# Optimization experiments

Measured on AMD Instinct MI355X. Metric: run time of the kernel, lower is better.

Reference implementation:

```python
import jax, jax.numpy as jnp
import numpy as np

G = 32          # grid size passed to FlashKAN
K_DEG = 3       # cubic B-splines
LO, HI = -3.0, 3.0

def make_knots():
    h = (HI - LO) / G
    # extended uniform knot vector: G + 2k + 1 knots -> G + k = 35 cubic basis fns
    return jnp.asarray(np.linspace(LO - K_DEG * h, HI + K_DEG * h, G + 2 * K_DEG + 1), jnp.float32)

def bspline_basis(x, knots):
    # Cox-de Boor, vectorized over all leading dims; loop only over degree (3 iters)
    xe = jnp.clip(x, LO, HI - 1e-4)[..., None]
    b = ((xe >= knots[:-1]) & (xe < knots[1:])).astype(x.dtype)  # degree-0 indicators
    for d in range(1, K_DEG + 1):
        left = (xe - knots[:-(d + 1)]) / (knots[d:-1] - knots[:-(d + 1)]) * b[..., :-1]
        right = (knots[d + 1:] - xe) / (knots[d + 1:] - knots[1:-d]) * b[..., 1:]
        b = left + right
    return b  # [..., E, G+K_DEG]

def kan(x, w_base, w_sp, knots):
    # FlashKAN layer: SiLU base branch + B-spline branch
    base = jax.nn.silu(x) @ w_base                          # [..., E] @ [E, O]
    spline = jnp.einsum('bleg,ego->blo', bspline_basis(x, knots), w_sp)
    return base + spline

def reference(query, key, value, wq_base, wq_sp, wk_base, wk_sp, wv_base, wv_sp):
    B, L, E = query.shape
    S = key.shape[-2]
    H = 8
    Dh = E // H
    knots = make_knots()
    Q = kan(query, wq_base, wq_sp, knots).reshape(B, L, H, Dh).transpose(0, 2, 1, 3)
    K = kan(key, wk_base, wk_sp, knots).reshape(B, S, H, Dh).transpose(0, 2, 1, 3)
    V = kan(value, wv_base, wv_sp, knots).reshape(B, S, H, Dh).transpose(0, 2, 1, 3)
    # no softmax, dropout p=0 -> (Q @ K^T) @ V == Q @ (K^T @ V), use O(L*d^2) form
    KtV = jnp.einsum('bhsd,bhse->bhde', K, V)               # [B,H,Dh,Dh]
    out = jnp.einsum('bhld,bhde->bhle', Q, KtV)             # [B,H,L,Dh]
    return out.transpose(0, 2, 1, 3).reshape(B, L, E)

def setup_inputs():
    key = jax.random.key(0)
    ks = jax.random.split(key, 9)
    B, L, E, NB = 2, 1024, 512, G + K_DEG
    sp_scale = 0.1 / np.sqrt(E)
    base_scale = 1.0 / np.sqrt(E)
    return {
        'query': jax.random.normal(ks[0], (B, L, E), jnp.float32),
        'key': jax.random.normal(ks[1], (B, L, E), jnp.float32),
        'value': jax.random.normal(ks[2], (B, L, E), jnp.float32),
        'wq_base': jax.random.normal(ks[3], (E, E), jnp.float32) * base_scale,
        'wq_sp': jax.random.normal(ks[4], (E, NB, E), jnp.float32) * sp_scale,
        'wk_base': jax.random.normal(ks[5], (E, E), jnp.float32) * base_scale,
        'wk_sp': jax.random.normal(ks[6], (E, NB, E), jnp.float32) * sp_scale,
        'wv_base': jax.random.normal(ks[7], (E, E), jnp.float32) * base_scale,
        'wv_sp': jax.random.normal(ks[8], (E, NB, E), jnp.float32) * sp_scale,
    }
```

## Files before the change

kernel.cpp:

```cpp
#include <hip/hip_runtime.h>
#include <hip/hip_bf16.h>
#include <stdint.h>

#define E_DIM 512
#define GNB   35
#define KSP   17920
#define KAUG  18432
#define MTOK  2048
#define BKW   128
#define NWIN  144
#define WINB  140
#define BM    128
#define BN    128

typedef __attribute__((ext_vector_type(8))) short  short8;
typedef __attribute__((ext_vector_type(4))) short  short4v;
typedef __attribute__((ext_vector_type(4))) float  floatx4;

__device__ __forceinline__ short f2bf(float f) {
  __hip_bfloat16 h = __float2bfloat16(f);
  return *reinterpret_cast<short*>(&h);
}
__device__ __forceinline__ float silu_f(float x) { return x / (1.0f + __expf(-x)); }

__device__ __forceinline__ void gload_lds16(const void* g, void* l) {
  typedef const __attribute__((address_space(1))) void* gp_t;
  typedef __attribute__((address_space(3))) void* lp_t;
  __builtin_amdgcn_global_load_lds((gp_t)g, (lp_t)l, 16, 0, 0);
}

__device__ __forceinline__ int kofs(int sl) { return ((sl >> 2) << 5) + ((sl & 3) << 3); }

__global__ __launch_bounds__(256) void wconv_kernel(
    const float* __restrict__ wq_sp, const float* __restrict__ wq_base,
    const float* __restrict__ wk_sp, const float* __restrict__ wk_base,
    const float* __restrict__ wv_sp, const float* __restrict__ wv_base,
    __hip_bfloat16* __restrict__ waugT)
{
  __shared__ float tile[64][65];
  const int tz = blockIdx.z;
  const float* wsp = tz == 0 ? wq_sp : (tz == 1 ? wk_sp : wv_sp);
  const float* wb  = tz == 0 ? wq_base : (tz == 1 ? wk_base : wv_base);
  const int k0 = blockIdx.x * 64;
  const int o0 = blockIdx.y * 64;
  const int t  = threadIdx.x;
  const float* srcb = (k0 < KSP) ? wsp + (size_t)k0 * E_DIM
                                 : wb + (size_t)(k0 - KSP) * E_DIM;
#pragma unroll
  for (int it = 0; it < 4; ++it) {
    int idx = it * 256 + t;
    int r = idx >> 4, c4 = (idx & 15) * 4;
    floatx4 v = *(const floatx4*)&srcb[(size_t)r * E_DIM + o0 + c4];
    tile[r][c4] = v.x; tile[r][c4 + 1] = v.y;
    tile[r][c4 + 2] = v.z; tile[r][c4 + 3] = v.w;
  }
  __syncthreads();
  __hip_bfloat16* dst = waugT + (size_t)tz * E_DIM * KAUG;
#pragma unroll
  for (int it = 0; it < 4; ++it) {
    int idx = it * 256 + t;
    int ro = idx >> 4, kc = (idx & 15) * 4;
    short4v s;
    s.x = f2bf(tile[kc][ro]);     s.y = f2bf(tile[kc + 1][ro]);
    s.z = f2bf(tile[kc + 2][ro]); s.w = f2bf(tile[kc + 3][ro]);
    *(short4v*)&dst[(size_t)(o0 + ro) * KAUG + k0 + kc] = s;
  }
}

template<int MODE>
__global__ __launch_bounds__(256) void kan_gemm(
    const float* __restrict__ q, const float* __restrict__ k_in,
    const float* __restrict__ v, const __hip_bfloat16* __restrict__ waugT,
    const float* __restrict__ wq_sp, const float* __restrict__ wq_base,
    const float* __restrict__ wk_sp, const float* __restrict__ wk_base,
    const float* __restrict__ wv_sp, const float* __restrict__ wv_base,
    float* __restrict__ C)
{
  __shared__ char pA[32768];
  __shared__ char pB[32768];

  const int bid = blockIdx.x;
  const int lid = (bid & 7) * 96 + (bid >> 3);
  const int mx = lid & 15;
  const int ny = (lid >> 4) & 3;
  const int z  = lid >> 6;
  const int tz = z >> 2;
  const int ks = z & 3;

  const float* X = tz == 0 ? q : (tz == 1 ? k_in : v);
  const float* Wsp = tz == 0 ? wq_sp : (tz == 1 ? wk_sp : wv_sp);
  const float* Wb  = tz == 0 ? wq_base : (tz == 1 ? wk_base : wv_base);
  const char* WTb = (const char*)(waugT + (size_t)tz * E_DIM * KAUG);
  float* Cout = C + (size_t)tz * MTOK * E_DIM;

  const int m0 = mx * BM;
  const int n0 = ny * BN;
  const int t = threadIdx.x;
  const int lane = t & 63, wid = t >> 6;
  const int wm = wid >> 1, wn = wid & 1;
  const int fr = lane & 15, kg = lane >> 4;

  floatx4 acc[4][4];
  const floatx4 zf = {0.f, 0.f, 0.f, 0.f};
#pragma unroll
  for (int i = 0; i < 4; ++i)
#pragma unroll
    for (int j = 0; j < 4; ++j) acc[i][j] = zf;

  const int colt = t & 127;
  const int slhi = t >> 7;

  const int w_lo = ks * (NWIN / 4), w_hi = w_lo + (NWIN / 4);
  for (int win = w_lo; win < w_hi; ++win) {
    const int k0 = win * BKW;
    const bool spline = (win < WINB);
    __syncthreads();

    if (MODE == 0) {
#pragma unroll
      for (int p = 0; p < 8; ++p) {
        const int sl = 2 * p + slhi;
        size_t goff = ((size_t)(n0 + colt) * KAUG + k0 + kofs(sl)) * 2;
        gload_lds16(WTb + goff, pB + p * 4096 + t * 16);
      }
    } else {
      const float* Wrow = spline ? Wsp : Wb;
      const int koff0 = spline ? k0 : k0 - KSP;
      const int g  = t & 31;
      const int rg = t >> 5;
#pragma unroll
      for (int p = 0; p < 4; ++p) {
        const int r0 = (p * 8 + rg) * 4;
        const int sl = ((r0 >> 5) << 2) | ((r0 >> 3) & 3);
        float rv[4][4];
#pragma unroll
        for (int j = 0; j < 4; ++j) {
          const float* src = &Wrow[(size_t)(koff0 + r0 + j) * E_DIM + n0 + g];
#pragma unroll
          for (int j2 = 0; j2 < 4; ++j2) rv[j][j2] = src[32 * j2];
        }
#pragma unroll
        for (int j2 = 0; j2 < 4; ++j2) {
          const int nloc = g + 32 * j2;
          short4v sv;
          sv.x = f2bf(rv[0][j2]); sv.y = f2bf(rv[1][j2]);
          sv.z = f2bf(rv[2][j2]); sv.w = f2bf(rv[3][j2]);
          *(short4v*)&pB[sl * 2048 + nloc * 16 + (r0 & 7) * 2] = sv;
        }
      }
    }

    if (spline) {
      const int4 z4 = make_int4(0, 0, 0, 0);
#pragma unroll
      for (int p = 0; p < 8; ++p) ((int4*)pA)[p * 256 + t] = z4;
      asm volatile("s_waitcnt lgkmcnt(0)" ::: "memory");
      __builtin_amdgcn_s_barrier();
      const int elo = k0 / GNB;
      int ehi = (k0 + BKW - 1) / GNB; if (ehi > 511) ehi = 511;
      const int ne = ehi - elo + 1;
      const int npairs = BM * ne;
      for (int p = t; p < npairs; p += 256) {
        int m, ei;
        if (ne == 4) { m = p >> 2; ei = p & 3; }
        else         { m = (p * 52429) >> 18; ei = p - m * 5; }
        const int e = elo + ei;
        float x = X[(size_t)(m0 + m) * E_DIM + e];
        x = fminf(fmaxf(x, -3.0f), 3.0f - 1e-4f);
        float u = (x + 3.0f) * (16.0f / 3.0f);
        int ii = (int)u; ii = ii > 31 ? 31 : ii;
        float tt = u - (float)ii;
        float omt = 1.0f - tt;
        float t2 = tt * tt, t3 = t2 * tt;
        float w4[4];
        w4[0] = omt * omt * omt * (1.0f / 6.0f);
        w4[1] = (3.0f * t3 - 6.0f * t2 + 4.0f) * (1.0f / 6.0f);
        w4[2] = (-3.0f * t3 + 3.0f * t2 + 3.0f * tt + 1.0f) * (1.0f / 6.0f);
        w4[3] = t3 * (1.0f / 6.0f);
        const int c = e * GNB + ii - k0;
#pragma unroll
        for (int j = 0; j < 4; ++j) {
          const int k = c + j;
          if (k >= 0 && k < BKW) {
            const int sl = ((k >> 5) << 2) | ((k >> 3) & 3);
            *(short*)&pA[sl * 2048 + m * 16 + (k & 7) * 2] = f2bf(w4[j]);
          }
        }
      }
    } else {
      const int e0 = k0 - KSP;
#pragma unroll
      for (int p = 0; p < 8; ++p) {
        const int id = p * 256 + t;
        const int m = id & 127, sl = id >> 7;
        const float* xs = &X[(size_t)(m0 + m) * E_DIM + e0 + kofs(sl)];
        floatx4 a = *(const floatx4*)xs;
        floatx4 b = *(const floatx4*)(xs + 4);
        short8 pk;
        pk[0] = f2bf(silu_f(a.x)); pk[1] = f2bf(silu_f(a.y));
        pk[2] = f2bf(silu_f(a.z)); pk[3] = f2bf(silu_f(a.w));
        pk[4] = f2bf(silu_f(b.x)); pk[5] = f2bf(silu_f(b.y));
        pk[6] = f2bf(silu_f(b.z)); pk[7] = f2bf(silu_f(b.w));
        *(short8*)&pA[sl * 2048 + m * 16] = pk;
      }
    }
    asm volatile("s_waitcnt vmcnt(0) lgkmcnt(0)" ::: "memory");
    __builtin_amdgcn_s_barrier();

    const int arow = (wm * 64 + fr) * 16;
    const int brow = (wn * 64 + fr) * 16;
    const int sbase = kg * 2048;
#pragma unroll
    for (int kc = 0; kc < 4; ++kc) {
      const int so = sbase + kc * 8192;
      short8 af[4], bfv[4];
#pragma unroll
      for (int fm = 0; fm < 4; ++fm)
        af[fm] = *(const short8*)&pA[so + arow + fm * 256];
#pragma unroll
      for (int fn = 0; fn < 4; ++fn)
        bfv[fn] = *(const short8*)&pB[so + brow + fn * 256];
#pragma unroll
      for (int fm = 0; fm < 4; ++fm)
#pragma unroll
        for (int fn = 0; fn < 4; ++fn)
          acc[fm][fn] = __builtin_amdgcn_mfma_f32_16x16x32_bf16(
              af[fm], bfv[fn], acc[fm][fn], 0, 0, 0);
    }
  }

  const int rowb = kg * 4;
#pragma unroll
  for (int fm = 0; fm < 4; ++fm)
#pragma unroll
    for (int fn = 0; fn < 4; ++fn)
#pragma unroll
      for (int r = 0; r < 4; ++r)
        atomicAdd(&Cout[(size_t)(m0 + wm * 64 + fm * 16 + rowb + r) * E_DIM
                        + (n0 + wn * 64 + fn * 16 + fr)],
                  acc[fm][fn][r]);
}

__global__ __launch_bounds__(256) void ktv_kernel(const float* __restrict__ C,
                                                  float* __restrict__ KtV)
{
  __shared__ float Ks[64][64];
  __shared__ float Vs[64][64];
  const int sc = blockIdx.x, bh = blockIdx.y;
  const int b = bh >> 3, h = bh & 7;
  const int t = threadIdx.x;
  const size_t base = ((size_t)(b * 1024 + sc * 64)) * E_DIM + h * 64;
  const float* Kp = C + (size_t)MTOK * E_DIM + base;
  const float* Vp = C + (size_t)2 * MTOK * E_DIM + base;
#pragma unroll
  for (int p = 0; p < 16; ++p) {
    int idx = p * 256 + t;
    int r = idx >> 6, c = idx & 63;
    Ks[r][c] = Kp[(size_t)r * E_DIM + c];
    Vs[r][c] = Vp[(size_t)r * E_DIM + c];
  }
  __syncthreads();
  const int d0 = (t & 15) * 4, e0 = (t >> 4) * 4;
  float acc[4][4] = {};
  for (int s = 0; s < 64; ++s) {
    float4 kv = *(const float4*)&Ks[s][d0];
    float4 vv = *(const float4*)&Vs[s][e0];
    float ka[4] = {kv.x, kv.y, kv.z, kv.w};
    float va[4] = {vv.x, vv.y, vv.z, vv.w};
#pragma unroll
    for (int i = 0; i < 4; ++i)
#pragma unroll
      for (int j = 0; j < 4; ++j) acc[i][j] = __fmaf_rn(ka[i], va[j], acc[i][j]);
  }
  float* dst = KtV + (size_t)bh * 4096;
#pragma unroll
  for (int i = 0; i < 4; ++i)
#pragma unroll
    for (int j = 0; j < 4; ++j)
      atomicAdd(&dst[(d0 + i) * 64 + (e0 + j)], acc[i][j]);
}

__global__ __launch_bounds__(256) void qktv_kernel(const float* __restrict__ C,
                                                   const float* __restrict__ KtV,
                                                   float* __restrict__ out)
{
  __shared__ float Qs[128][64];
  __shared__ float Ms[64][64];
  const int lt = blockIdx.x, bh = blockIdx.y;
  const int b = bh >> 3, h = bh & 7;
  const int t = threadIdx.x;
  const float* Qp = C + ((size_t)(b * 1024 + lt * 128)) * E_DIM + h * 64;
#pragma unroll
  for (int p = 0; p < 32; ++p) {
    int idx = p * 256 + t;
    Qs[idx >> 6][idx & 63] = Qp[(size_t)(idx >> 6) * E_DIM + (idx & 63)];
  }
#pragma unroll
  for (int p = 0; p < 16; ++p) {
    int idx = p * 256 + t;
    Ms[idx >> 6][idx & 63] = KtV[(size_t)bh * 4096 + idx];
  }
  __syncthreads();
  const int e0 = (t & 15) * 4;
  const int l0 = (t >> 4) * 8;
  float acc[8][4] = {};
  for (int d = 0; d < 64; ++d) {
    float4 mv = *(const float4*)&Ms[d][e0];
    float ma[4] = {mv.x, mv.y, mv.z, mv.w};
#pragma unroll
    for (int i = 0; i < 8; ++i) {
      float qv = Qs[l0 + i][d];
#pragma unroll
      for (int j = 0; j < 4; ++j) acc[i][j] = __fmaf_rn(qv, ma[j], acc[i][j]);
    }
  }
  float* op = out + ((size_t)(b * 1024 + lt * 128)) * E_DIM + h * 64;
#pragma unroll
  for (int i = 0; i < 8; ++i)
#pragma unroll
    for (int j = 0; j < 4; ++j)
      op[(size_t)(l0 + i) * E_DIM + (e0 + j)] = acc[i][j];
}

extern "C" void kernel_launch(void* const* d_in, const int* in_sizes, int n_in,
                              void* d_out, int out_size, void* d_ws, size_t ws_size,
                              hipStream_t stream) {
  const float* q   = (const float*)d_in[0];
  const float* k   = (const float*)d_in[1];
  const float* v   = (const float*)d_in[2];
  const float* wqb = (const float*)d_in[3];
  const float* wqs = (const float*)d_in[4];
  const float* wkb = (const float*)d_in[5];
  const float* wks = (const float*)d_in[6];
  const float* wvb = (const float*)d_in[7];
  const float* wvs = (const float*)d_in[8];

  char* ws = (char*)d_ws;
  const size_t WAUG_BYTES = (size_t)3 * E_DIM * KAUG * sizeof(__hip_bfloat16);
  const size_t C_BYTES    = (size_t)3 * MTOK * E_DIM * sizeof(float);
  const size_t KTV_BYTES  = (size_t)16 * 64 * 64 * sizeof(float);
  const bool full = ws_size >= WAUG_BYTES + C_BYTES + KTV_BYTES;

  float* C;
  float* KtV;
  __hip_bfloat16* waugT = (__hip_bfloat16*)ws;
  if (full) { C = (float*)(ws + WAUG_BYTES); KtV = (float*)(ws + WAUG_BYTES + C_BYTES); }
  else      { C = (float*)ws;                KtV = (float*)(ws + C_BYTES); }

  hipMemsetAsync(C, 0, C_BYTES, stream);
  hipMemsetAsync(KtV, 0, KTV_BYTES, stream);

  if (full) {
    wconv_kernel<<<dim3(KAUG / 64, E_DIM / 64, 3), 256, 0, stream>>>(
        wqs, wqb, wks, wkb, wvs, wvb, waugT);
    kan_gemm<0><<<dim3(768), 256, 0, stream>>>(
        q, k, v, waugT, wqs, wqb, wks, wkb, wvs, wvb, C);
  } else {
    kan_gemm<1><<<dim3(768), 256, 0, stream>>>(
        q, k, v, waugT, wqs, wqb, wks, wkb, wvs, wvb, C);
  }
  ktv_kernel<<<dim3(16, 16), 256, 0, stream>>>(C, KtV);
  qktv_kernel<<<dim3(8, 16), 256, 0, stream>>>(C, KtV, (float*)d_out);
}
```

Baseline: 440.8 us.

## Drop weight pre-conversion pass and software-pipeline KAN GEMM with double-buffered LDS

```diff
diff --git a/kernel.cpp b/kernel.cpp
--- a/kernel.cpp
+++ b/kernel.cpp
@@ -7,14 +7,13 @@
 #define KSP   17920
 #define KAUG  18432
 #define MTOK  2048
-#define BKW   128
-#define NWIN  144
-#define WINB  140
+#define BKW   64
+#define NWIN  288
+#define WINB  280
 #define BM    128
 #define BN    128
 
 typedef __attribute__((ext_vector_type(8))) short  short8;
-typedef __attribute__((ext_vector_type(4))) short  short4v;
 typedef __attribute__((ext_vector_type(4))) float  floatx4;
 
 __device__ __forceinline__ short f2bf(float f) {
@@ -23,61 +22,17 @@
 }
 __device__ __forceinline__ float silu_f(float x) { return x / (1.0f + __expf(-x)); }
 
-__device__ __forceinline__ void gload_lds16(const void* g, void* l) {
-  typedef const __attribute__((address_space(1))) void* gp_t;
-  typedef __attribute__((address_space(3))) void* lp_t;
-  __builtin_amdgcn_global_load_lds((gp_t)g, (lp_t)l, 16, 0, 0);
-}
-
 __device__ __forceinline__ int kofs(int sl) { return ((sl >> 2) << 5) + ((sl & 3) << 3); }
 
-__global__ __launch_bounds__(256) void wconv_kernel(
-    const float* __restrict__ wq_sp, const float* __restrict__ wq_base,
-    const float* __restrict__ wk_sp, const float* __restrict__ wk_base,
-    const float* __restrict__ wv_sp, const float* __restrict__ wv_base,
-    __hip_bfloat16* __restrict__ waugT)
-{
-  __shared__ float tile[64][65];
-  const int tz = blockIdx.z;
-  const float* wsp = tz == 0 ? wq_sp : (tz == 1 ? wk_sp : wv_sp);
-  const float* wb  = tz == 0 ? wq_base : (tz == 1 ? wk_base : wv_base);
-  const int k0 = blockIdx.x * 64;
-  const int o0 = blockIdx.y * 64;
-  const int t  = threadIdx.x;
-  const float* srcb = (k0 < KSP) ? wsp + (size_t)k0 * E_DIM
-                                 : wb + (size_t)(k0 - KSP) * E_DIM;
-#pragma unroll
-  for (int it = 0; it < 4; ++it) {
-    int idx = it * 256 + t;
-    int r = idx >> 4, c4 = (idx & 15) * 4;
-    floatx4 v = *(const floatx4*)&srcb[(size_t)r * E_DIM + o0 + c4];
-    tile[r][c4] = v.x; tile[r][c4 + 1] = v.y;
-    tile[r][c4 + 2] = v.z; tile[r][c4 + 3] = v.w;
-  }
-  __syncthreads();
-  __hip_bfloat16* dst = waugT + (size_t)tz * E_DIM * KAUG;
-#pragma unroll
-  for (int it = 0; it < 4; ++it) {
-    int idx = it * 256 + t;
-    int ro = idx >> 4, kc = (idx & 15) * 4;
-    short4v s;
-    s.x = f2bf(tile[kc][ro]);     s.y = f2bf(tile[kc + 1][ro]);
-    s.z = f2bf(tile[kc + 2][ro]); s.w = f2bf(tile[kc + 3][ro]);
-    *(short4v*)&dst[(size_t)(o0 + ro) * KAUG + k0 + kc] = s;
-  }
-}
-
-template<int MODE>
-__global__ __launch_bounds__(256) void kan_gemm(
+__global__ __launch_bounds__(256, 2) void kan_gemm(
     const float* __restrict__ q, const float* __restrict__ k_in,
-    const float* __restrict__ v, const __hip_bfloat16* __restrict__ waugT,
+    const float* __restrict__ v,
     const float* __restrict__ wq_sp, const float* __restrict__ wq_base,
     const float* __restrict__ wk_sp, const float* __restrict__ wk_base,
     const float* __restrict__ wv_sp, const float* __restrict__ wv_base,
     float* __restrict__ C)
 {
-  __shared__ char pA[32768];
-  __shared__ char pB[32768];
+  __shared__ char lds[65536];
 
   const int bid = blockIdx.x;
   const int lid = (bid & 7) * 96 + (bid >> 3);
@@ -87,10 +42,9 @@
   const int tz = z >> 2;
   const int ks = z & 3;
 
-  const float* X = tz == 0 ? q : (tz == 1 ? k_in : v);
+  const float* X   = tz == 0 ? q : (tz == 1 ? k_in : v);
   const float* Wsp = tz == 0 ? wq_sp : (tz == 1 ? wk_sp : wv_sp);
   const float* Wb  = tz == 0 ? wq_base : (tz == 1 ? wk_base : wv_base);
-  const char* WTb = (const char*)(waugT + (size_t)tz * E_DIM * KAUG);
   float* Cout = C + (size_t)tz * MTOK * E_DIM;
 
   const int m0 = mx * BM;
@@ -99,6 +53,7 @@
   const int lane = t & 63, wid = t >> 6;
   const int wm = wid >> 1, wn = wid & 1;
   const int fr = lane & 15, kg = lane >> 4;
+  const int gB = t & 31, slB = t >> 5;
 
   floatx4 acc[4][4];
   const floatx4 zf = {0.f, 0.f, 0.f, 0.f};
@@ -107,119 +62,157 @@
 #pragma unroll
     for (int j = 0; j < 4; ++j) acc[i][j] = zf;
 
-  const int colt = t & 127;
-  const int slhi = t >> 7;
-
   const int w_lo = ks * (NWIN / 4), w_hi = w_lo + (NWIN / 4);
-  for (int win = w_lo; win < w_hi; ++win) {
-    const int k0 = win * BKW;
-    const bool spline = (win < WINB);
-    __syncthreads();
-
-    if (MODE == 0) {
-#pragma unroll
-      for (int p = 0; p < 8; ++p) {
-        const int sl = 2 * p + slhi;
-        size_t goff = ((size_t)(n0 + colt) * KAUG + k0 + kofs(sl)) * 2;
-        gload_lds16(WTb + goff, pB + p * 4096 + t * 16);
-      }
-    } else {
-      const float* Wrow = spline ? Wsp : Wb;
-      const int koff0 = spline ? k0 : k0 - KSP;
-      const int g  = t & 31;
-      const int rg = t >> 5;
-#pragma unroll
-      for (int p = 0; p < 4; ++p) {
-        const int r0 = (p * 8 + rg) * 4;
-        const int sl = ((r0 >> 5) << 2) | ((r0 >> 3) & 3);
-        float rv[4][4];
-#pragma unroll
-        for (int j = 0; j < 4; ++j) {
-          const float* src = &Wrow[(size_t)(koff0 + r0 + j) * E_DIM + n0 + g];
-#pragma unroll
-          for (int j2 = 0; j2 < 4; ++j2) rv[j][j2] = src[32 * j2];
-        }
-#pragma unroll
-        for (int j2 = 0; j2 < 4; ++j2) {
-          const int nloc = g + 32 * j2;
-          short4v sv;
-          sv.x = f2bf(rv[0][j2]); sv.y = f2bf(rv[1][j2]);
-          sv.z = f2bf(rv[2][j2]); sv.w = f2bf(rv[3][j2]);
-          *(short4v*)&pB[sl * 2048 + nloc * 16 + (r0 & 7) * 2] = sv;
-        }
-      }
-    }
-
-    if (spline) {
-      const int4 z4 = make_int4(0, 0, 0, 0);
-#pragma unroll
-      for (int p = 0; p < 8; ++p) ((int4*)pA)[p * 256 + t] = z4;
-      asm volatile("s_waitcnt lgkmcnt(0)" ::: "memory");
-      __builtin_amdgcn_s_barrier();
-      const int elo = k0 / GNB;
-      int ehi = (k0 + BKW - 1) / GNB; if (ehi > 511) ehi = 511;
-      const int ne = ehi - elo + 1;
-      const int npairs = BM * ne;
-      for (int p = t; p < npairs; p += 256) {
-        int m, ei;
-        if (ne == 4) { m = p >> 2; ei = p & 3; }
-        else         { m = (p * 52429) >> 18; ei = p - m * 5; }
-        const int e = elo + ei;
-        float x = X[(size_t)(m0 + m) * E_DIM + e];
-        x = fminf(fmaxf(x, -3.0f), 3.0f - 1e-4f);
-        float u = (x + 3.0f) * (16.0f / 3.0f);
-        int ii = (int)u; ii = ii > 31 ? 31 : ii;
-        float tt = u - (float)ii;
-        float omt = 1.0f - tt;
-        float t2 = tt * tt, t3 = t2 * tt;
-        float w4[4];
-        w4[0] = omt * omt * omt * (1.0f / 6.0f);
-        w4[1] = (3.0f * t3 - 6.0f * t2 + 4.0f) * (1.0f / 6.0f);
-        w4[2] = (-3.0f * t3 + 3.0f * t2 + 3.0f * tt + 1.0f) * (1.0f / 6.0f);
-        w4[3] = t3 * (1.0f / 6.0f);
-        const int c = e * GNB + ii - k0;
-#pragma unroll
-        for (int j = 0; j < 4; ++j) {
-          const int k = c + j;
-          if (k >= 0 && k < BKW) {
-            const int sl = ((k >> 5) << 2) | ((k >> 3) & 3);
-            *(short*)&pA[sl * 2048 + m * 16 + (k & 7) * 2] = f2bf(w4[j]);
-          }
-        }
-      }
-    } else {
-      const int e0 = k0 - KSP;
-#pragma unroll
-      for (int p = 0; p < 8; ++p) {
-        const int id = p * 256 + t;
-        const int m = id & 127, sl = id >> 7;
-        const float* xs = &X[(size_t)(m0 + m) * E_DIM + e0 + kofs(sl)];
-        floatx4 a = *(const floatx4*)xs;
-        floatx4 b = *(const floatx4*)(xs + 4);
-        short8 pk;
-        pk[0] = f2bf(silu_f(a.x)); pk[1] = f2bf(silu_f(a.y));
-        pk[2] = f2bf(silu_f(a.z)); pk[3] = f2bf(silu_f(a.w));
-        pk[4] = f2bf(silu_f(b.x)); pk[5] = f2bf(silu_f(b.y));
-        pk[6] = f2bf(silu_f(b.z)); pk[7] = f2bf(silu_f(b.w));
-        *(short8*)&pA[sl * 2048 + m * 16] = pk;
-      }
-    }
-    asm volatile("s_waitcnt vmcnt(0) lgkmcnt(0)" ::: "memory");
-    __builtin_amdgcn_s_barrier();
+
+  float rv[32];
+  float xc[2], xn[2];
+
+#define WPAR(warg, k0v, elov, nev)                                  \
+  const int k0v = (warg) * BKW;                                     \
+  const int elov = k0v / GNB;                                       \
+  int ehi_ = (k0v + BKW - 1) / GNB; if (ehi_ > 511) ehi_ = 511;     \
+  const int nev = ehi_ - elov + 1;
+
+#define ISSUE_B(warg)                                                          \
+  {                                                                            \
+    const int k0w = (warg) * BKW;                                              \
+    const float* src = (warg) < WINB ? Wsp + (size_t)k0w * E_DIM               \
+                                     : Wb + (size_t)(k0w - KSP) * E_DIM;       \
+    const float* srow = src + (size_t)kofs(slB) * E_DIM + n0 + gB;             \
+    _Pragma("unroll")                                                          \
+    for (int j = 0; j < 8; ++j)                                                \
+      _Pragma("unroll")                                                        \
+      for (int i = 0; i < 4; ++i)                                              \
+        rv[j * 4 + i] = srow[(size_t)j * E_DIM + 32 * i];                      \
+  }
+
+#define WRITE_B(Bb)                                                            \
+  {                                                                            \
+    _Pragma("unroll")                                                          \
+    for (int i = 0; i < 4; ++i) {                                              \
+      short8 s;                                                                \
+      _Pragma("unroll")                                                        \
+      for (int j = 0; j < 8; ++j) s[j] = f2bf(rv[j * 4 + i]);                  \
+      *(short8*)((Bb) + slB * 2048 + (gB + 32 * i) * 16) = s;                  \
+    }                                                                          \
+  }
+
+#define PREF_X(warg, xp)                                                       \
+  {                                                                            \
+    WPAR(warg, k0w, elow, new_)                                                \
+    (void)k0w;                                                                 \
+    _Pragma("unroll")                                                          \
+    for (int idx = 0; idx < 2; ++idx) {                                        \
+      const int p = t + idx * 256;                                             \
+      if (p < 128 * new_)                                                      \
+        xp[idx] = X[(size_t)(m0 + (p & 127)) * E_DIM + elow + (p >> 7)];       \
+    }                                                                          \
+  }
+
+#define ZERO_A(Ab)                                                             \
+  {                                                                            \
+    const int4 z4 = make_int4(0, 0, 0, 0);                                     \
+    _Pragma("unroll")                                                          \
+    for (int p = 0; p < 4; ++p) ((int4*)(Ab))[p * 256 + t] = z4;               \
+  }
+
+#define SCATTER_A(warg, Ab, xp)                                                \
+  {                                                                            \
+    WPAR(warg, k0w, elow, new_)                                                \
+    _Pragma("unroll")                                                          \
+    for (int idx = 0; idx < 2; ++idx) {                                        \
+      const int p = t + idx * 256;                                             \
+      if (p < 128 * new_) {                                                    \
+        const int m = p & 127, e = elow + (p >> 7);                            \
+        float x = fminf(fmaxf(xp[idx], -3.0f), 3.0f - 1e-4f);                  \
+        float u = (x + 3.0f) * (16.0f / 3.0f);                                 \
+        int ii = (int)u; ii = ii > 31 ? 31 : ii;                               \
+        float tt = u - (float)ii, omt = 1.0f - tt;                             \
+        float t2 = tt * tt, t3 = t2 * tt;                                      \
+        float w4[4];                                                           \
+        w4[0] = omt * omt * omt * (1.0f / 6.0f);                               \
+        w4[1] = (3.0f * t3 - 6.0f * t2 + 4.0f) * (1.0f / 6.0f);                \
+        w4[2] = (-3.0f * t3 + 3.0f * t2 + 3.0f * tt + 1.0f) * (1.0f / 6.0f);   \
+        w4[3] = t3 * (1.0f / 6.0f);                                            \
+        const int kbase = e * GNB + ii - k0w;                                  \
+        _Pragma("unroll")                                                      \
+        for (int j = 0; j < 4; ++j) {                                          \
+          const int kk = kbase + j;                                            \
+          if ((unsigned)kk < BKW) {                                            \
+            const int sl = ((kk >> 5) << 2) | ((kk >> 3) & 3);                 \
+            *(short*)((Ab) + sl * 2048 + m * 16 + (kk & 7) * 2) = f2bf(w4[j]); \
+          }                                                                    \
+        }                                                                      \
+      }                                                                        \
+    }                                                                          \
+  }
+
+#define BASE_A(warg, Ab)                                                       \
+  {                                                                            \
+    const int e0w = (warg) * BKW - KSP;                                        \
+    _Pragma("unroll")                                                          \
+    for (int it = 0; it < 4; ++it) {                                           \
+      const int c = it * 256 + t;                                              \
+      const int m = c & 127, sl = c >> 7;                                      \
+      const float* xs = &X[(size_t)(m0 + m) * E_DIM + e0w + kofs(sl)];         \
+      floatx4 av = *(const floatx4*)xs;                                        \
+      floatx4 bv = *(const floatx4*)(xs + 4);                                  \
+      short8 pk;                                                               \
+      pk[0] = f2bf(silu_f(av[0])); pk[1] = f2bf(silu_f(av[1]));                \
+      pk[2] = f2bf(silu_f(av[2])); pk[3] = f2bf(silu_f(av[3]));                \
+      pk[4] = f2bf(silu_f(bv[0])); pk[5] = f2bf(silu_f(bv[1]));                \
+      pk[6] = f2bf(silu_f(bv[2])); pk[7] = f2bf(silu_f(bv[3]));                \
+      *(short8*)((Ab) + sl * 2048 + m * 16) = pk;                              \
+    }                                                                          \
+  }
+
+#define LGKM_BAR()                                                             \
+  asm volatile("s_waitcnt lgkmcnt(0)" ::: "memory");                           \
+  __builtin_amdgcn_s_barrier();
+
+  {
+    ISSUE_B(w_lo);
+    PREF_X(w_lo, xc);
+    PREF_X(w_lo + 1, xn);
+    char* Ab = lds + (w_lo & 1) * 16384;
+    char* Bb = lds + 32768 + (w_lo & 1) * 16384;
+    ZERO_A(Ab);
+    LGKM_BAR();
+    SCATTER_A(w_lo, Ab, xc);
+    WRITE_B(Bb);
+  }
+
+  for (int w = w_lo; w < w_hi; ++w) {
+    LGKM_BAR();
+
+    const int wn1 = (w + 1 < w_hi) ? w + 1 : w_hi - 1;
+    const int wn2 = (w + 2 < w_hi) ? w + 2 : w_hi - 1;
+    const int pn = (w + 1) & 1;
+    char* Acur = lds + (w & 1) * 16384;
+    char* Bcur = lds + 32768 + (w & 1) * 16384;
+    char* Anxt = lds + pn * 16384;
+    char* Bnxt = lds + 32768 + pn * 16384;
+
+    ISSUE_B(wn1);
+    xc[0] = xn[0]; xc[1] = xn[1];
+    if (wn2 < WINB) { PREF_X(wn2, xn); }
+    if (wn1 < WINB) { ZERO_A(Anxt); }
+
+    LGKM_BAR();
 
     const int arow = (wm * 64 + fr) * 16;
     const int brow = (wn * 64 + fr) * 16;
     const int sbase = kg * 2048;
 #pragma unroll
-    for (int kc = 0; kc < 4; ++kc) {
+    for (int kc = 0; kc < 2; ++kc) {
       const int so = sbase + kc * 8192;
       short8 af[4], bfv[4];
 #pragma unroll
       for (int fm = 0; fm < 4; ++fm)
-        af[fm] = *(const short8*)&pA[so + arow + fm * 256];
+        af[fm] = *(const short8*)(Acur + so + arow + fm * 256);
 #pragma unroll
       for (int fn = 0; fn < 4; ++fn)
-        bfv[fn] = *(const short8*)&pB[so + brow + fn * 256];
+        bfv[fn] = *(const short8*)(Bcur + so + brow + fn * 256);
 #pragma unroll
       for (int fm = 0; fm < 4; ++fm)
 #pragma unroll
@@ -227,6 +220,10 @@
           acc[fm][fn] = __builtin_amdgcn_mfma_f32_16x16x32_bf16(
               af[fm], bfv[fn], acc[fm][fn], 0, 0, 0);
     }
+
+    if (wn1 < WINB) { SCATTER_A(wn1, Anxt, xc); }
+    else            { BASE_A(wn1, Anxt); }
+    WRITE_B(Bnxt);
   }
 
   const int rowb = kg * 4;
@@ -336,29 +333,16 @@
   const float* wvs = (const float*)d_in[8];
 
   char* ws = (char*)d_ws;
-  const size_t WAUG_BYTES = (size_t)3 * E_DIM * KAUG * sizeof(__hip_bfloat16);
-  const size_t C_BYTES    = (size_t)3 * MTOK * E_DIM * sizeof(float);
-  const size_t KTV_BYTES  = (size_t)16 * 64 * 64 * sizeof(float);
-  const bool full = ws_size >= WAUG_BYTES + C_BYTES + KTV_BYTES;
-
-  float* C;
-  float* KtV;
-  __hip_bfloat16* waugT = (__hip_bfloat16*)ws;
-  if (full) { C = (float*)(ws + WAUG_BYTES); KtV = (float*)(ws + WAUG_BYTES + C_BYTES); }
-  else      { C = (float*)ws;                KtV = (float*)(ws + C_BYTES); }
-
-  hipMemsetAsync(C, 0, C_BYTES, stream);
-  hipMemsetAsync(KtV, 0, KTV_BYTES, stream);
-
-  if (full) {
-    wconv_kernel<<<dim3(KAUG / 64, E_DIM / 64, 3), 256, 0, stream>>>(
-        wqs, wqb, wks, wkb, wvs, wvb, waugT);
-    kan_gemm<0><<<dim3(768), 256, 0, stream>>>(
-        q, k, v, waugT, wqs, wqb, wks, wkb, wvs, wvb, C);
-  } else {
-    kan_gemm<1><<<dim3(768), 256, 0, stream>>>(
-        q, k, v, waugT, wqs, wqb, wks, wkb, wvs, wvb, C);
-  }
+  const size_t C_BYTES   = (size_t)3 * MTOK * E_DIM * sizeof(float);
+  const size_t KTV_BYTES = (size_t)16 * 64 * 64 * sizeof(float);
+  float* C   = (float*)ws;
+  float* KtV = (float*)(ws + C_BYTES);
+
+  (void)hipMemsetAsync(C, 0, C_BYTES, stream);
+  (void)hipMemsetAsync(KtV, 0, KTV_BYTES, stream);
+
+  kan_gemm<<<dim3(768), 256, 0, stream>>>(
+      q, k, v, wqs, wqb, wks, wkb, wvs, wvb, C);
   ktv_kernel<<<dim3(16, 16), 256, 0, stream>>>(C, KtV);
   qktv_kernel<<<dim3(8, 16), 256, 0, stream>>>(C, KtV, (float*)d_out);
 }
```

New measurement: 402.2 us. 8.8% less time.
